# Optimization experiments

Measured on AMD Instinct MI355X. Metric: run time of the kernel, lower is better.

The kernel has to match this reference:

```python
import jax, jax.numpy as jnp
import numpy as np

EMB = 256
HEADS = 4
HD = EMB // HEADS
BS, SZ = 4, 64


def _layernorm(x, g, b, eps=1e-5):
    mu = jnp.mean(x, axis=-1, keepdims=True)
    var = jnp.mean((x - mu) ** 2, axis=-1, keepdims=True)
    return (x - mu) * jax.lax.rsqrt(var + eps) * g + b


def setup_inputs() -> dict:
    key = jax.random.key(0)
    ks = jax.random.split(key, 12)
    s = lambda k, shape, sc: jax.random.normal(k, shape, jnp.float32) * sc
    return {
        "x": s(ks[0], (BS, EMB, SZ, SZ), 1.0),
        "ln1_g": jnp.ones((EMB,), jnp.float32),
        "ln1_b": jnp.zeros((EMB,), jnp.float32),
        "wq": s(ks[1], (HD, HD), HD ** -0.5), "bq": jnp.zeros((HD,), jnp.float32),
        "wk": s(ks[2], (HD, HD), HD ** -0.5), "bk": jnp.zeros((HD,), jnp.float32),
        "wv": s(ks[3], (HD, HD), HD ** -0.5), "bv": jnp.zeros((HD,), jnp.float32),
        "wo": s(ks[4], (EMB, EMB), EMB ** -0.5), "bo": jnp.zeros((EMB,), jnp.float32),
        "ln2_g": jnp.ones((EMB,), jnp.float32),
        "ln2_b": jnp.zeros((EMB,), jnp.float32),
        "w1": s(ks[5], (EMB, EMB), EMB ** -0.5), "b1": jnp.zeros((EMB,), jnp.float32),
        "w2": s(ks[6], (EMB, EMB), EMB ** -0.5), "b2": jnp.zeros((EMB,), jnp.float32),
    }


def reference(x, ln1_g, ln1_b, wq, bq, wk, bk, wv, bv, wo, bo, ln2_g, ln2_b, w1, b1, w2, b2):
    bs, c, sz, _ = x.shape
    seq = sz * sz
    xt = x.reshape(bs, c, seq).swapaxes(1, 2)  # [b, s, c]
    xn = _layernorm(xt, ln1_g, ln1_b)
    # split heads: [b, h, s, d]
    h = xn.reshape(bs, seq, HEADS, HD).transpose(0, 2, 1, 3)
    q = h @ wq + bq
    k = h @ wk + bk
    v = h @ wv + bv
    scores = jnp.einsum("bhqd,bhkd->bhqk", q, k) / (HD ** 0.5)
    attn = jax.nn.softmax(scores, axis=-1)
    o = jnp.einsum("bhqk,bhkd->bhqd", attn, v)
    o = o.transpose(0, 2, 1, 3).reshape(bs, seq, c)
    o = o @ wo + bo
    av = o + xt  # residual 1
    ff = _layernorm(av, ln2_g, ln2_b) @ w1 + b1
    ff = jax.nn.gelu(ff, approximate=False) @ w2 + b2
    out = ff + av  # residual 2
    return out.swapaxes(1, 2).reshape(bs, c, sz, sz)
```

## Files before the change

### kernel.cpp

```cpp
#include <hip/hip_runtime.h>
#include <hip/hip_bf16.h>
#include <cstdint>

typedef __attribute__((ext_vector_type(8))) short short8;
typedef __attribute__((ext_vector_type(4))) short short4_;
typedef __attribute__((ext_vector_type(4))) float float4_;
typedef __attribute__((ext_vector_type(16))) float f32x16;

#define MFMA16(a,b,c)  __builtin_amdgcn_mfma_f32_16x16x32_bf16(a,b,c,0,0,0)
#define MFMA32(a,b,c)  __builtin_amdgcn_mfma_f32_32x32x16_bf16(a,b,c,0,0,0)
#define EXP2(x) __builtin_amdgcn_exp2f(x)

__device__ __forceinline__ short f2bs(float f) {
    union { float f; uint32_t u; } c;
    c.f = f;
    c.u += 0x7FFF + ((c.u >> 16) & 1);
    return (short)(c.u >> 16);
}
__device__ __forceinline__ float s2f(short s) {
    union { uint32_t u; float f; } c;
    c.u = ((uint32_t)(uint16_t)s) << 16;
    return c.f;
}

static const int EMB = 256;
static const int SEQ = 4096;
static const int TOK = 16384;

static const size_t SZO = 4194304;
static const size_t LSTRIDE = 65536;

#define QSCALE 0.18033688011112042f

__global__ __launch_bounds__(256) void repack_kernel(
    const float* wq, const float* wk, const float* wv,
    const float* wo, const float* w1, const float* w2,
    short* wqT, short* wkT, short* wvT, short* woT, short* w1T, short* w2T)
{
    int idx = blockIdx.x * 256 + threadIdx.x;
    if (idx < 3 * 4096) {
        int m = idx / 4096, r = idx % 4096;
        int n = r / 64, k = r % 64;
        const float* src = (m == 0) ? wq : (m == 1) ? wk : wv;
        short* dst = (m == 0) ? wqT : (m == 1) ? wkT : wvT;
        float v = src[k * 64 + n];
        if (m == 0) v *= QSCALE;
        dst[n * 64 + k] = f2bs(v);
    } else {
        int idx2 = idx - 3 * 4096;
        if (idx2 < 3 * 65536) {
            int m = idx2 / 65536, r = idx2 % 65536;
            int n = r / 256, k = r % 256;
            const float* src = (m == 0) ? wo : (m == 1) ? w1 : w2;
            short* dst = (m == 0) ? woT : (m == 1) ? w1T : w2T;
            dst[n * 256 + k] = f2bs(src[k * 256 + n]);
        }
    }
}

__global__ __launch_bounds__(256) void ln1_kernel(
    const float* x, const float* g, const float* bta,
    short* xn, short* xt)
{
    __shared__ float redS[4][32], redQ[4][32];
    int tid = threadIdx.x;
    int l = tid & 31;
    int p = tid >> 5;
    int t = blockIdx.x * 32 + l;
    int b = t >> 12, sp = t & 4095;
    const float* xb = x + (size_t)b * EMB * SEQ + (size_t)(p * 32) * SEQ + sp;

    float v[32];
    float sum = 0.f, ss = 0.f;
#pragma unroll
    for (int j = 0; j < 32; j++) {
        v[j] = xb[(size_t)j * SEQ];
        sum += v[j]; ss += v[j] * v[j];
    }
    sum += __shfl_xor(sum, 32);
    ss  += __shfl_xor(ss, 32);
    int w = tid >> 6;
    if ((tid & 32) == 0) { redS[w][l] = sum; redQ[w][l] = ss; }
    __syncthreads();
    float S = (redS[0][l] + redS[1][l]) + (redS[2][l] + redS[3][l]);
    float Q = (redQ[0][l] + redQ[1][l]) + (redQ[2][l] + redQ[3][l]);
    float mu = S * (1.f / 256.f);
    float var = Q * (1.f / 256.f) - mu * mu;
    float rs = rsqrtf(var + 1e-5f);

    short* xnr = xn + (size_t)t * 256 + p * 32;
    short* xtr = xt + (size_t)t * 256 + p * 32;
#pragma unroll
    for (int c = 0; c < 32; c += 8) {
        short8 ra, na;
#pragma unroll
        for (int j = 0; j < 8; j++) {
            float vv = v[c + j];
            ra[j] = f2bs(vv);
            na[j] = f2bs((vv - mu) * rs * g[p * 32 + c + j] + bta[p * 32 + c + j]);
        }
        *(short8*)(xtr + c) = ra;
        *(short8*)(xnr + c) = na;
    }
}

__global__ __launch_bounds__(256) void qkv_kernel(
    const short* xn, const short* wqT, const short* wkT, const short* wvT,
    const float* bq, const float* bk, const float* bv,
    short* qo, short* ko, short* vto)
{
    int tid = threadIdx.x;
    int w = tid >> 6, lane = tid & 63, quad = lane >> 4, l15 = lane & 15;
    int m0 = blockIdx.x * 64 + w * 16;
    int row = m0 + l15;
    int bb = row >> 12;
    int s0 = (m0 & 4095) + quad * 4;

    short8 a0[4], a1[4];
#pragma unroll
    for (int h = 0; h < 4; h++) {
        a0[h] = *(const short8*)(xn + (size_t)row * 256 + h * 64 + quad * 8);
        a1[h] = *(const short8*)(xn + (size_t)row * 256 + h * 64 + 32 + quad * 8);
    }

#pragma unroll
    for (int p = 0; p < 3; p++) {
        const short* WT = (p == 0) ? wqT : (p == 1) ? wkT : wvT;
        const float* bias = (p == 0) ? bq : (p == 1) ? bk : bv;
        float bscale = (p == 0) ? QSCALE : 1.f;
#pragma unroll
        for (int nb = 0; nb < 4; nb++) {
            int col = nb * 16 + l15;
            short8 b0 = *(const short8*)(WT + col * 64 + quad * 8);
            short8 b1 = *(const short8*)(WT + col * 64 + 32 + quad * 8);
            float bvv = bias[col] * bscale;
#pragma unroll
            for (int h = 0; h < 4; h++) {
                float4_ acc = {bvv, bvv, bvv, bvv};
                acc = MFMA16(a0[h], b0, acc);
                acc = MFMA16(a1[h], b1, acc);
                size_t headbase = (size_t)(bb * 4 + h) * SEQ;
                if (p < 2) {
                    short* dst = (p == 0) ? qo : ko;
#pragma unroll
                    for (int r = 0; r < 4; r++)
                        dst[(headbase + s0 + r) * 64 + col] = f2bs(acc[r]);
                } else {
                    short4_ pk;
#pragma unroll
                    for (int r = 0; r < 4; r++) pk[r] = f2bs(acc[r]);
                    *(short4_*)(vto + ((size_t)(bb * 4 + h) * 64 + col) * SEQ + s0) = pk;
                }
            }
        }
    }
}

__global__ __attribute__((amdgpu_flat_work_group_size(256, 256),
                          amdgpu_waves_per_eu(4, 4)))
void flash_kernel(
    const short* q, const short* k, const short* vt,
    short* O0, short* Orest, float* lbase)
{
    __shared__ short K_lds[64 * 64];
    __shared__ short V_lds[64 * 64];

    int tid = threadIdx.x;
    int w = tid >> 6, lane = tid & 63;
    int l31 = lane & 31, hh = lane >> 5, l7 = l31 & 7;
    int qt = blockIdx.x, bh = blockIdx.y, grp = blockIdx.z;
    int span = 64 / gridDim.z;

    const short* qb = q + (size_t)bh * SEQ * 64;
    const short* kb = k + (size_t)bh * SEQ * 64 + (size_t)grp * span * 64 * 64;
    const short* vb = vt + (size_t)bh * 64 * SEQ + grp * span * 64;

    int qrow = qt * 128 + w * 32 + l31;
    short8 qf[4];
#pragma unroll
    for (int kb4 = 0; kb4 < 4; kb4++)
        qf[kb4] = *(const short8*)(qb + (size_t)qrow * 64 + kb4 * 16 + hh * 8);

    f32x16 oacc[2];
#pragma unroll
    for (int td = 0; td < 2; td++)
#pragma unroll
        for (int i = 0; i < 16; i++) oacc[td][i] = 0.f;
    float li = 0.f;

    int srow = tid >> 2;
    int sr7 = srow & 7;
    int c0 = tid & 3;
    int dcA = (c0 ^ sr7) << 3;
    int dcB = ((c0 + 4) ^ sr7) << 3;

    short8 kr0 = *(const short8*)(kb + (size_t)srow * 64 + c0 * 8);
    short8 kr1 = *(const short8*)(kb + (size_t)srow * 64 + (c0 + 4) * 8);
    short8 vr0 = *(const short8*)(vb + (size_t)srow * SEQ + c0 * 8);
    short8 vr1 = *(const short8*)(vb + (size_t)srow * SEQ + (c0 + 4) * 8);

    for (int kt = 0; kt < span; kt++) {
        __syncthreads();
        *(short8*)&K_lds[srow * 64 + dcA] = kr0;
        *(short8*)&K_lds[srow * 64 + dcB] = kr1;
        *(short8*)&V_lds[srow * 64 + dcA] = vr0;
        *(short8*)&V_lds[srow * 64 + dcB] = vr1;
        if (kt + 1 < span) {
            kr0 = *(const short8*)(kb + (size_t)((kt + 1) * 64 + srow) * 64 + c0 * 8);
            kr1 = *(const short8*)(kb + (size_t)((kt + 1) * 64 + srow) * 64 + (c0 + 4) * 8);
            vr0 = *(const short8*)(vb + (size_t)srow * SEQ + (kt + 1) * 64 + c0 * 8);
            vr1 = *(const short8*)(vb + (size_t)srow * SEQ + (kt + 1) * 64 + (c0 + 4) * 8);
        }
        asm volatile("s_waitcnt lgkmcnt(0)" ::: "memory");
        __builtin_amdgcn_s_barrier();
        asm volatile("" ::: "memory");

#pragma unroll
        for (int t = 0; t < 2; t++) {
            f32x16 acc;
#pragma unroll
            for (int i = 0; i < 16; i++) acc[i] = 0.f;
#pragma unroll
            for (int kb4 = 0; kb4 < 4; kb4++) {
                short8 ka = *(const short8*)&K_lds[(t * 32 + l31) * 64 +
                                                   (((kb4 * 2 + hh) ^ l7) << 3)];
                acc = MFMA32(ka, qf[kb4], acc);
            }
#pragma unroll
            for (int i = 0; i < 16; i++) acc[i] = EXP2(acc[i]);
            li += ((acc[0] + acc[1]) + (acc[2] + acc[3]))
                + ((acc[4] + acc[5]) + (acc[6] + acc[7]))
                + ((acc[8] + acc[9]) + (acc[10] + acc[11]))
                + ((acc[12] + acc[13]) + (acc[14] + acc[15]));
            short8 wf[2];
#pragma unroll
            for (int kbl = 0; kbl < 2; kbl++) {
                uint32_t A0, A1, B0, B1;
                asm("v_cvt_pk_bf16_f32 %0, %1, %2" : "=v"(A0)
                    : "v"(acc[kbl * 8 + 0]), "v"(acc[kbl * 8 + 1]));
                asm("v_cvt_pk_bf16_f32 %0, %1, %2" : "=v"(A1)
                    : "v"(acc[kbl * 8 + 2]), "v"(acc[kbl * 8 + 3]));
                asm("v_cvt_pk_bf16_f32 %0, %1, %2" : "=v"(B0)
                    : "v"(acc[kbl * 8 + 4]), "v"(acc[kbl * 8 + 5]));
                asm("v_cvt_pk_bf16_f32 %0, %1, %2" : "=v"(B1)
                    : "v"(acc[kbl * 8 + 6]), "v"(acc[kbl * 8 + 7]));
                asm("v_permlane32_swap_b32 %0, %1" : "+v"(A0), "+v"(B0));
                asm("v_permlane32_swap_b32 %0, %1" : "+v"(A1), "+v"(B1));
                union { short8 s; uint32_t u[4]; } pw;
                pw.u[0] = A0; pw.u[1] = A1; pw.u[2] = B0; pw.u[3] = B1;
                wf[kbl] = pw.s;
            }
            __builtin_amdgcn_s_setprio(1);
#pragma unroll
            for (int kbl = 0; kbl < 2; kbl++) {
                int kc = (t * 2 + kbl) * 2 + hh;
#pragma unroll
                for (int td = 0; td < 2; td++) {
                    short8 va = *(const short8*)&V_lds[(td * 32 + l31) * 64 +
                                                       ((kc ^ l7) << 3)];
                    oacc[td] = MFMA32(va, wf[kbl], oacc[td]);
                }
            }
            __builtin_amdgcn_s_setprio(0);
        }
    }

    li += __shfl_xor(li, 32);

    short* Op = grp ? (Orest + (size_t)(grp - 1) * SZO) : O0;
    float* lp = lbase + (size_t)grp * LSTRIDE;
    if (hh == 0) lp[bh * 4096 + qrow] = li;

    size_t ob = ((size_t)bh * 4096 + qrow) * 64;
#pragma unroll
    for (int td = 0; td < 2; td++)
#pragma unroll
        for (int g = 0; g < 4; g++) {
            short4_ pk;
#pragma unroll
            for (int r = 0; r < 4; r++) pk[r] = f2bs(oacc[td][g * 4 + r]);
            *(short4_*)(Op + ob + td * 32 + g * 8 + hh * 4) = pk;
        }
}

__global__ __launch_bounds__(256) void combine_kernel(
    const short* O0, const short* Orest, const float* lb,
    short* Oout, int np)
{
    int g = blockIdx.x * 256 + threadIdx.x;
    int qi = g >> 4;
    short4_ a = *(const short4_*)(O0 + (size_t)g * 4);
    float l = lb[qi];
    float4_ acc = {s2f(a[0]), s2f(a[1]), s2f(a[2]), s2f(a[3])};
    for (int j = 1; j < np; j++) {
        short4_ b = *(const short4_*)(Orest + (size_t)(j - 1) * SZO + (size_t)g * 4);
        l += lb[(size_t)j * LSTRIDE + qi];
#pragma unroll
        for (int jj = 0; jj < 4; jj++) acc[jj] += s2f(b[jj]);
    }
    float inv = 1.f / l;
    short4_ pk;
#pragma unroll
    for (int j = 0; j < 4; j++) pk[j] = f2bs(acc[j] * inv);
    *(short4_*)(Oout + (size_t)g * 4) = pk;
}

__global__ __launch_bounds__(256) void mlp_kernel(
    const short* O0, const short* Orest, const float* lb, int np,
    const short* woT, const short* w1T, const short* w2T,
    const float* bo, const float* b1, const float* b2,
    const float* g2, const float* be2,
    const short* xt, float* outf)
{
    __shared__ __align__(16) char smem[3 * 8448 + 128];
    short* av = (short*)smem;
    short* x2 = (short*)(smem + 8448);
    short* ff = (short*)(smem + 16896);
    float* stats = (float*)(smem + 25344);
    float* T = (float*)smem;

    int tid = threadIdx.x;
    int w = tid >> 6, lane = tid & 63, quad = lane >> 4, l15 = lane & 15;
    int m0 = blockIdx.x * 16;
    int n0 = w * 64;
    int arow = m0 + l15;
    int bbA = arow >> 12, spA = arow & 4095;

    float invh[4];
    if (np) {
#pragma unroll
        for (int h = 0; h < 4; h++) {
            size_t li = (size_t)(bbA * 4 + h) * 4096 + spA;
            float s = lb[li];
            for (int j = 1; j < np; j++) s += lb[(size_t)j * LSTRIDE + li];
            invh[h] = 1.f / s;
        }
    }

    float4_ acc[4];
#pragma unroll
    for (int nb = 0; nb < 4; nb++) {
        float bvv = bo[n0 + nb * 16 + l15];
        acc[nb] = {bvv, bvv, bvv, bvv};
    }
    for (int kc = 0; kc < 8; kc++) {
        int h = kc >> 1;
        int off = (kc & 1) * 32 + quad * 8;
        size_t obase = ((size_t)(bbA * 4 + h) * 4096 + spA) * 64 + off;
        short8 a;
        if (np) {
            short8 a0v = *(const short8*)(O0 + obase);
            float f[8];
#pragma unroll
            for (int jj = 0; jj < 8; jj++) f[jj] = s2f(a0v[jj]);
            for (int j = 1; j < np; j++) {
                short8 apv = *(const short8*)(Orest + (size_t)(j - 1) * SZO + obase);
#pragma unroll
                for (int jj = 0; jj < 8; jj++) f[jj] += s2f(apv[jj]);
            }
            float iv = invh[h];
            union { short8 s; uint32_t u[4]; } pa;
#pragma unroll
            for (int jj = 0; jj < 4; jj++) {
                float f0 = f[2 * jj] * iv;
                float f1 = f[2 * jj + 1] * iv;
                asm("v_cvt_pk_bf16_f32 %0, %1, %2" : "=v"(pa.u[jj]) : "v"(f0), "v"(f1));
            }
            a = pa.s;
        } else {
            a = *(const short8*)(O0 + obase);
        }
#pragma unroll
        for (int nb = 0; nb < 4; nb++) {
            short8 b = *(const short8*)(woT + (size_t)(n0 + nb * 16 + l15) * 256 + kc * 32 + quad * 8);
            acc[nb] = MFMA16(a, b, acc[nb]);
        }
    }
#pragma unroll
    for (int nb = 0; nb < 4; nb++) {
        int col = n0 + nb * 16 + l15;
#pragma unroll
        for (int r = 0; r < 4; r++) {
            size_t t = (size_t)m0 + quad * 4 + r;
            av[(quad * 4 + r) * 264 + col] = f2bs(acc[nb][r] + s2f(xt[t * 256 + col]));
        }
    }
    __syncthreads();

    {
        int row = tid >> 4, sub = tid & 15;
        float sum = 0.f, ss = 0.f;
        short8 v0 = *(const short8*)&av[row * 264 + sub * 16];
        short8 v1 = *(const short8*)&av[row * 264 + sub * 16 + 8];
#pragma unroll
        for (int j = 0; j < 8; j++) {
            float a = s2f(v0[j]), b = s2f(v1[j]);
            sum += a + b; ss += a * a + b * b;
        }
#pragma unroll
        for (int off = 1; off < 16; off <<= 1) {
            sum += __shfl_xor(sum, off);
            ss += __shfl_xor(ss, off);
        }
        if (sub == 0) {
            float mu = sum * (1.f / 256.f);
            float var = ss * (1.f / 256.f) - mu * mu;
            stats[row] = mu;
            stats[16 + row] = rsqrtf(var + 1e-5f);
        }
    }
    __syncthreads();

    {
        int row = tid >> 4, sub = tid & 15;
        float mu = stats[row], rs = stats[16 + row];
#pragma unroll
        for (int j = 0; j < 16; j += 4) {
            int c = sub * 16 + j;
            short4_ rv = *(const short4_*)&av[row * 264 + c];
            short4_ pk;
#pragma unroll
            for (int i = 0; i < 4; i++)
                pk[i] = f2bs((s2f(rv[i]) - mu) * rs * g2[c + i] + be2[c + i]);
            *(short4_*)&x2[row * 264 + c] = pk;
        }
    }
    __syncthreads();

#pragma unroll
    for (int nb = 0; nb < 4; nb++) {
        float bvv = b1[n0 + nb * 16 + l15];
        acc[nb] = {bvv, bvv, bvv, bvv};
    }
    for (int kc = 0; kc < 8; kc++) {
        short8 a = *(const short8*)&x2[l15 * 264 + kc * 32 + quad * 8];
#pragma unroll
        for (int nb = 0; nb < 4; nb++) {
            short8 b = *(const short8*)(w1T + (size_t)(n0 + nb * 16 + l15) * 256 + kc * 32 + quad * 8);
            acc[nb] = MFMA16(a, b, acc[nb]);
        }
    }
#pragma unroll
    for (int nb = 0; nb < 4; nb++) {
        int col = n0 + nb * 16 + l15;
#pragma unroll
        for (int r = 0; r < 4; r++) {
            float v = acc[nb][r];
            v = 0.5f * v * (1.f + erff(v * 0.70710678118f));
            ff[(quad * 4 + r) * 264 + col] = f2bs(v);
        }
    }
    __syncthreads();

#pragma unroll
    for (int nb = 0; nb < 4; nb++) {
        float bvv = b2[n0 + nb * 16 + l15];
        acc[nb] = {bvv, bvv, bvv, bvv};
    }
    for (int kc = 0; kc < 8; kc++) {
        short8 a = *(const short8*)&ff[l15 * 264 + kc * 32 + quad * 8];
#pragma unroll
        for (int nb = 0; nb < 4; nb++) {
            short8 b = *(const short8*)(w2T + (size_t)(n0 + nb * 16 + l15) * 256 + kc * 32 + quad * 8);
            acc[nb] = MFMA16(a, b, acc[nb]);
        }
    }
    float vout[4][4];
#pragma unroll
    for (int nb = 0; nb < 4; nb++) {
        int col = n0 + nb * 16 + l15;
#pragma unroll
        for (int r = 0; r < 4; r++)
            vout[nb][r] = acc[nb][r] + s2f(av[(quad * 4 + r) * 264 + col]);
    }
    __syncthreads();

    float* tw = T + w * 1040;
#pragma unroll
    for (int nb = 0; nb < 4; nb++)
#pragma unroll
        for (int r = 0; r < 4; r++)
            tw[(quad * 4 + r) * 65 + nb * 16 + l15] = vout[nb][r];

    int bb = m0 >> 12;
    int spb = m0 & 4095;
    float* dst = outf + ((size_t)bb * 256 + n0 + lane) * SEQ + spb;
#pragma unroll
    for (int j = 0; j < 16; j += 4) {
        float4_ pk = {tw[(j + 0) * 65 + lane], tw[(j + 1) * 65 + lane],
                      tw[(j + 2) * 65 + lane], tw[(j + 3) * 65 + lane]};
        *(float4_*)(dst + j) = pk;
    }
}

extern "C" void kernel_launch(void* const* d_in, const int* in_sizes, int n_in,
                              void* d_out, int out_size, void* d_ws, size_t ws_size,
                              hipStream_t stream)
{
    const float* x     = (const float*)d_in[0];
    const float* ln1_g = (const float*)d_in[1];
    const float* ln1_b = (const float*)d_in[2];
    const float* wq    = (const float*)d_in[3];
    const float* bq    = (const float*)d_in[4];
    const float* wk    = (const float*)d_in[5];
    const float* bk    = (const float*)d_in[6];
    const float* wv    = (const float*)d_in[7];
    const float* bv    = (const float*)d_in[8];
    const float* wo    = (const float*)d_in[9];
    const float* bo    = (const float*)d_in[10];
    const float* ln2_g = (const float*)d_in[11];
    const float* ln2_b = (const float*)d_in[12];
    const float* w1    = (const float*)d_in[13];
    const float* b1    = (const float*)d_in[14];
    const float* w2    = (const float*)d_in[15];
    const float* b2    = (const float*)d_in[16];

    char* ws = (char*)d_ws;
    const size_t SZ_BF = (size_t)TOK * 256 * 2;

    short* wqT = (short*)(ws + 0);
    short* wkT = (short*)(ws + 8192);
    short* wvT = (short*)(ws + 16384);
    short* woT = (short*)(ws + 24576);
    short* w1T = (short*)(ws + 155648);
    short* w2T = (short*)(ws + 286720);
    char* base = ws + 524288;

    short* xt  = (short*)(base);
    short* kbuf= (short*)(base + SZ_BF);
    short* vtb = (short*)(base + 2 * SZ_BF);

    const size_t need2_fb = 524288 + 3 * SZ_BF + 524288 + SZ_BF;
    const size_t need2_fu = need2_fb + SZ_BF;
    const size_t need4_fb = 524288 + 3 * SZ_BF + 1048576 + 3 * SZ_BF;
    const size_t need4_fu = need4_fb + SZ_BF;

    int nz, fuse;
    if (ws_size >= need4_fb)      { nz = 4; fuse = (ws_size >= need4_fu); }
    else if (ws_size >= need2_fb) { nz = 2; fuse = (ws_size >= need2_fu); }
    else                          { nz = 1; fuse = 0; }

    float* lbase;
    short* Orest;
    short* O0w;
    if (nz == 4) {
        lbase = (float*)(base + 3 * SZ_BF);
        Orest = (short*)(base + 3 * SZ_BF + 1048576);
        O0w   = Orest + 3 * SZO;
    } else {
        lbase = (float*)(base + 3 * SZ_BF);
        Orest = (short*)(base + 3 * SZ_BF + 524288);
        O0w   = Orest + SZO;
    }

    short* qb  = (short*)d_out;
    short* xn  = (short*)((char*)d_out + SZ_BF);
    short* O0  = fuse ? O0w : xn;
    short* Onrm= vtb;

    repack_kernel<<<816, 256, 0, stream>>>(wq, wk, wv, wo, w1, w2,
                                           wqT, wkT, wvT, woT, w1T, w2T);
    ln1_kernel<<<TOK / 32, 256, 0, stream>>>(x, ln1_g, ln1_b, xn, xt);
    qkv_kernel<<<TOK / 64, 256, 0, stream>>>(xn, wqT, wkT, wvT, bq, bk, bv,
                                             qb, kbuf, vtb);
    flash_kernel<<<dim3(32, 16, nz), 256, 0, stream>>>(qb, kbuf, vtb, O0, Orest, lbase);
    if (fuse) {
        mlp_kernel<<<TOK / 16, 256, 0, stream>>>(O0, Orest, lbase, nz,
                                                 woT, w1T, w2T, bo, b1, b2,
                                                 ln2_g, ln2_b, xt, (float*)d_out);
    } else {
        combine_kernel<<<4096, 256, 0, stream>>>(O0, Orest, lbase, Onrm, nz);
        mlp_kernel<<<TOK / 16, 256, 0, stream>>>(Onrm, Orest, lbase, 0,
                                                 woT, w1T, w2T, bo, b1, b2,
                                                 ln2_g, ln2_b, xt, (float*)d_out);
    }
}
```

Before: 298.0 us.

## Fuse LayerNorm1 into QKV projection via LDS and retune flash swizzle

Merges the ln1 and qkv kernels into one, so the normalized activations stay in padded shared memory instead of being written to and reread from global memory. The V projection now swaps MFMA operands so the transposed V output is written with lanes contiguous along the sequence axis. The flash kernel gets a new LDS XOR swizzle meant to reduce bank conflicts, and its waves_per_eu lower bound is relaxed from 4 to 2. The fused kernel holds 64 floats per thread and about 34 KB of LDS, which may lower occupancy.

```diff
diff --git a/kernel.cpp b/kernel.cpp
--- a/kernel.cpp
+++ b/kernel.cpp
@@ -58,29 +58,32 @@
     }
 }
 
-__global__ __launch_bounds__(256) void ln1_kernel(
+__global__ __attribute__((amdgpu_flat_work_group_size(256, 256),
+                          amdgpu_waves_per_eu(1, 4)))
+void ln1qkv_kernel(
     const float* x, const float* g, const float* bta,
-    short* xn, short* xt)
+    const short* wqT, const short* wkT, const short* wvT,
+    const float* bq, const float* bk, const float* bv,
+    short* xt, short* qo, short* ko, short* vto)
 {
-    __shared__ float redS[4][32], redQ[4][32];
+    __shared__ short xn_lds[64 * 264];
+    __shared__ float redS[4][64], redQ[4][64];
+
     int tid = threadIdx.x;
-    int l = tid & 31;
-    int p = tid >> 5;
-    int t = blockIdx.x * 32 + l;
+    int l = tid & 63;
+    int cp = tid >> 6;
+    int t = blockIdx.x * 64 + l;
     int b = t >> 12, sp = t & 4095;
-    const float* xb = x + (size_t)b * EMB * SEQ + (size_t)(p * 32) * SEQ + sp;
-
-    float v[32];
+    const float* xb = x + (size_t)b * EMB * SEQ + (size_t)(cp * 64) * SEQ + sp;
+
+    float v[64];
+#pragma unroll
+    for (int j = 0; j < 64; j++) v[j] = xb[(size_t)j * SEQ];
     float sum = 0.f, ss = 0.f;
 #pragma unroll
-    for (int j = 0; j < 32; j++) {
-        v[j] = xb[(size_t)j * SEQ];
-        sum += v[j]; ss += v[j] * v[j];
-    }
-    sum += __shfl_xor(sum, 32);
-    ss  += __shfl_xor(ss, 32);
-    int w = tid >> 6;
-    if ((tid & 32) == 0) { redS[w][l] = sum; redQ[w][l] = ss; }
+    for (int j = 0; j < 64; j++) { sum += v[j]; ss += v[j] * v[j]; }
+    redS[cp][l] = sum;
+    redQ[cp][l] = ss;
     __syncthreads();
     float S = (redS[0][l] + redS[1][l]) + (redS[2][l] + redS[3][l]);
     float Q = (redQ[0][l] + redQ[1][l]) + (redQ[2][l] + redQ[3][l]);
@@ -88,76 +91,88 @@
     float var = Q * (1.f / 256.f) - mu * mu;
     float rs = rsqrtf(var + 1e-5f);
 
-    short* xnr = xn + (size_t)t * 256 + p * 32;
-    short* xtr = xt + (size_t)t * 256 + p * 32;
-#pragma unroll
-    for (int c = 0; c < 32; c += 8) {
+    short* xtr = xt + (size_t)t * 256 + cp * 64;
+    short* xnr = xn_lds + l * 264 + cp * 64;
+#pragma unroll
+    for (int c = 0; c < 64; c += 8) {
         short8 ra, na;
 #pragma unroll
         for (int j = 0; j < 8; j++) {
             float vv = v[c + j];
             ra[j] = f2bs(vv);
-            na[j] = f2bs((vv - mu) * rs * g[p * 32 + c + j] + bta[p * 32 + c + j]);
+            na[j] = f2bs((vv - mu) * rs * g[cp * 64 + c + j] + bta[cp * 64 + c + j]);
         }
         *(short8*)(xtr + c) = ra;
         *(short8*)(xnr + c) = na;
     }
-}
-
-__global__ __launch_bounds__(256) void qkv_kernel(
-    const short* xn, const short* wqT, const short* wkT, const short* wvT,
-    const float* bq, const float* bk, const float* bv,
-    short* qo, short* ko, short* vto)
-{
-    int tid = threadIdx.x;
+    __syncthreads();
+
     int w = tid >> 6, lane = tid & 63, quad = lane >> 4, l15 = lane & 15;
     int m0 = blockIdx.x * 64 + w * 16;
     int row = m0 + l15;
     int bb = row >> 12;
-    int s0 = (m0 & 4095) + quad * 4;
-
+
+    const short* arow = xn_lds + (w * 16 + l15) * 264;
     short8 a0[4], a1[4];
 #pragma unroll
     for (int h = 0; h < 4; h++) {
-        a0[h] = *(const short8*)(xn + (size_t)row * 256 + h * 64 + quad * 8);
-        a1[h] = *(const short8*)(xn + (size_t)row * 256 + h * 64 + 32 + quad * 8);
+        a0[h] = *(const short8*)(arow + h * 64 + quad * 8);
+        a1[h] = *(const short8*)(arow + h * 64 + 32 + quad * 8);
     }
 
 #pragma unroll
     for (int p = 0; p < 3; p++) {
         const short* WT = (p == 0) ? wqT : (p == 1) ? wkT : wvT;
         const float* bias = (p == 0) ? bq : (p == 1) ? bk : bv;
-        float bscale = (p == 0) ? QSCALE : 1.f;
-#pragma unroll
-        for (int nb = 0; nb < 4; nb++) {
-            int col = nb * 16 + l15;
-            short8 b0 = *(const short8*)(WT + col * 64 + quad * 8);
-            short8 b1 = *(const short8*)(WT + col * 64 + 32 + quad * 8);
-            float bvv = bias[col] * bscale;
-#pragma unroll
-            for (int h = 0; h < 4; h++) {
-                float4_ acc = {bvv, bvv, bvv, bvv};
-                acc = MFMA16(a0[h], b0, acc);
-                acc = MFMA16(a1[h], b1, acc);
-                size_t headbase = (size_t)(bb * 4 + h) * SEQ;
-                if (p < 2) {
-                    short* dst = (p == 0) ? qo : ko;
+
+        if (p < 2) {
+            float bscale = (p == 0) ? QSCALE : 1.f;
+            short* dst = (p == 0) ? qo : ko;
+            int s0 = (m0 & 4095) + quad * 4;
+#pragma unroll
+            for (int nb = 0; nb < 4; nb++) {
+                int col = nb * 16 + l15;
+                short8 b0 = *(const short8*)(WT + col * 64 + quad * 8);
+                short8 b1 = *(const short8*)(WT + col * 64 + 32 + quad * 8);
+                float bvv = bias[col] * bscale;
+#pragma unroll
+                for (int h = 0; h < 4; h++) {
+                    float4_ acc = {bvv, bvv, bvv, bvv};
+                    acc = MFMA16(a0[h], b0, acc);
+                    acc = MFMA16(a1[h], b1, acc);
+                    size_t headbase = (size_t)(bb * 4 + h) * SEQ;
 #pragma unroll
                     for (int r = 0; r < 4; r++)
                         dst[(headbase + s0 + r) * 64 + col] = f2bs(acc[r]);
-                } else {
-                    short4_ pk;
-#pragma unroll
-                    for (int r = 0; r < 4; r++) pk[r] = f2bs(acc[r]);
-                    *(short4_*)(vto + ((size_t)(bb * 4 + h) * 64 + col) * SEQ + s0) = pk;
                 }
             }
+        } else {
+            int sp0 = m0 & 4095;
+#pragma unroll
+            for (int nb = 0; nb < 4; nb++) {
+                int colw = nb * 16 + l15;
+                short8 b0 = *(const short8*)(WT + colw * 64 + quad * 8);
+                short8 b1 = *(const short8*)(WT + colw * 64 + 32 + quad * 8);
+                float4_ binit;
+#pragma unroll
+                for (int r = 0; r < 4; r++) binit[r] = bias[nb * 16 + quad * 4 + r];
+#pragma unroll
+                for (int h = 0; h < 4; h++) {
+                    float4_ acc = binit;
+                    acc = MFMA16(b0, a0[h], acc);
+                    acc = MFMA16(b1, a1[h], acc);
+                    size_t dbase = ((size_t)(bb * 4 + h) * 64 + nb * 16 + quad * 4) * SEQ;
+#pragma unroll
+                    for (int r = 0; r < 4; r++)
+                        vto[dbase + (size_t)r * SEQ + sp0 + l15] = f2bs(acc[r]);
+                }
+            }
         }
     }
 }
 
 __global__ __attribute__((amdgpu_flat_work_group_size(256, 256),
-                          amdgpu_waves_per_eu(4, 4)))
+                          amdgpu_waves_per_eu(2, 4)))
 void flash_kernel(
     const short* q, const short* k, const short* vt,
     short* O0, short* Orest, float* lbase)
@@ -167,7 +182,7 @@
 
     int tid = threadIdx.x;
     int w = tid >> 6, lane = tid & 63;
-    int l31 = lane & 31, hh = lane >> 5, l7 = l31 & 7;
+    int l31 = lane & 31, hh = lane >> 5;
     int qt = blockIdx.x, bh = blockIdx.y, grp = blockIdx.z;
     int span = 64 / gridDim.z;
 
@@ -189,10 +204,12 @@
     float li = 0.f;
 
     int srow = tid >> 2;
-    int sr7 = srow & 7;
     int c0 = tid & 3;
-    int dcA = (c0 ^ sr7) << 3;
-    int dcB = ((c0 + 4) ^ sr7) << 3;
+    int sw = (srow & 7) ^ ((srow & 1) << 2);
+    int rw = (l31 & 7) ^ ((l31 & 1) << 2);
+
+    int dcA = (c0 ^ sw) << 3;
+    int dcB = ((c0 + 4) ^ sw) << 3;
 
     short8 kr0 = *(const short8*)(kb + (size_t)srow * 64 + c0 * 8);
     short8 kr1 = *(const short8*)(kb + (size_t)srow * 64 + (c0 + 4) * 8);
@@ -223,7 +240,7 @@
 #pragma unroll
             for (int kb4 = 0; kb4 < 4; kb4++) {
                 short8 ka = *(const short8*)&K_lds[(t * 32 + l31) * 64 +
-                                                   (((kb4 * 2 + hh) ^ l7) << 3)];
+                                                   (((kb4 * 2 + hh) ^ rw) << 3)];
                 acc = MFMA32(ka, qf[kb4], acc);
             }
 #pragma unroll
@@ -257,7 +274,7 @@
 #pragma unroll
                 for (int td = 0; td < 2; td++) {
                     short8 va = *(const short8*)&V_lds[(td * 32 + l31) * 64 +
-                                                       ((kc ^ l7) << 3)];
+                                                       ((kc ^ rw) << 3)];
                     oacc[td] = MFMA32(va, wf[kbl], oacc[td]);
                 }
             }
@@ -554,15 +571,15 @@
     }
 
     short* qb  = (short*)d_out;
-    short* xn  = (short*)((char*)d_out + SZ_BF);
-    short* O0  = fuse ? O0w : xn;
+    short* upper = (short*)((char*)d_out + SZ_BF);
+    short* O0  = fuse ? O0w : upper;
     short* Onrm= vtb;
 
     repack_kernel<<<816, 256, 0, stream>>>(wq, wk, wv, wo, w1, w2,
                                            wqT, wkT, wvT, woT, w1T, w2T);
-    ln1_kernel<<<TOK / 32, 256, 0, stream>>>(x, ln1_g, ln1_b, xn, xt);
-    qkv_kernel<<<TOK / 64, 256, 0, stream>>>(xn, wqT, wkT, wvT, bq, bk, bv,
-                                             qb, kbuf, vtb);
+    ln1qkv_kernel<<<TOK / 64, 256, 0, stream>>>(x, ln1_g, ln1_b,
+                                                wqT, wkT, wvT, bq, bk, bv,
+                                                xt, qb, kbuf, vtb);
     flash_kernel<<<dim3(32, 16, nz), 256, 0, stream>>>(qb, kbuf, vtb, O0, Orest, lbase);
     if (fuse) {
         mlp_kernel<<<TOK / 16, 256, 0, stream>>>(O0, Orest, lbase, nz,
```

Result: faster. 260.8 us (-12.5%).
